# Kernel tuning notes

Hardware: AMD Instinct MI355X
Metric: run time of the kernel (lower is better)

Reference implementation:

```python
import jax, jax.numpy as jnp
import numpy as np

EMB = 1024
NHEAD = 16
HEAD_DIM = EMB // NHEAD  # 64
L = 2048
NEG = -1e30


def setup_inputs() -> dict:
    key = jax.random.key(0)
    ks = jax.random.split(key, 8)
    # xavier_uniform bound for square [EMB, EMB] matrices
    bound = float(np.sqrt(6.0 / (EMB + EMB)))
    def xavier(k):
        return jax.random.uniform(k, (EMB, EMB), jnp.float32, -bound, bound)
    return {
        "q": jax.random.normal(ks[0], (L, EMB), jnp.float32),
        "k": jax.random.normal(ks[1], (L, EMB), jnp.float32),
        "v": jax.random.normal(ks[2], (L, EMB), jnp.float32),
        "mask": jax.random.randint(ks[3], (NHEAD, L, L), 0, 2) > 0,
        "Wq": xavier(ks[4]),
        "Wk": xavier(ks[5]),
        "Wv": xavier(ks[6]),
        "Wo": xavier(ks[7]),
    }


def reference(q, k, v, mask, Wq, Wk, Wv, Wo):
    scaling = HEAD_DIM ** -0.5
    # F.linear(x, W) = x @ W.T ; reshape to [H, L, D]
    Q = (q @ Wq.T).reshape(L, NHEAD, HEAD_DIM).swapaxes(0, 1)
    K = (k @ Wk.T).reshape(L, NHEAD, HEAD_DIM).swapaxes(0, 1)
    V = (v @ Wv.T).reshape(L, NHEAD, HEAD_DIM).swapaxes(0, 1)
    scores = jnp.einsum("hld,hmd->hlm", Q, K) * scaling  # [H, L, L]
    scores = jnp.where(mask, jnp.asarray(NEG, scores.dtype), scores)
    p = jax.nn.softmax(scores, axis=-1)
    # attn_mask=True: multiplicative re-mask after softmax (custom path)
    p = p * (~mask).astype(p.dtype)
    # dropout is a no-op in eval mode
    attn_out = jnp.einsum("hlm,hmd->hld", p, V)  # [H, L, D]
    attn_out = attn_out.swapaxes(0, 1).reshape(L, EMB)
    return attn_out @ Wo.T
```

## Files before the change

### kernel.cpp

```cpp
#include <hip/hip_runtime.h>
#include <stdint.h>

#define EMB   1024
#define NHEAD 16
#define HDIM  64
#define SEQ   2048

typedef unsigned short ushort_t;
typedef unsigned int   uint32;
typedef __attribute__((ext_vector_type(8))) short bfrag;
typedef __attribute__((ext_vector_type(4))) float ffrag;

#define MFMA(a, b, c) __builtin_amdgcn_mfma_f32_16x16x32_bf16((a), (b), (c), 0, 0, 0)

__device__ inline ushort_t f2bf(float f) {
  uint32 u = __float_as_uint(f);
  u += 0x7FFFu + ((u >> 16) & 1u);
  return (ushort_t)(u >> 16);
}
__device__ inline uint32 pack2(float a, float b) {
  return (uint32)f2bf(a) | ((uint32)f2bf(b) << 16);
}

__device__ inline void glds16(const ushort_t* g, ushort_t* l) {
  __builtin_amdgcn_global_load_lds(
      (const __attribute__((address_space(1))) uint32*)(uintptr_t)g,
      (__attribute__((address_space(3))) uint32*)(uintptr_t)l, 16, 0, 0);
}

__global__ void detect_mask_kernel(const uint32* __restrict__ mw, int* __restrict__ flag) {
  uint32 w = mw[threadIdx.x];
  bool is4 = (w == 0u) || (w == 1u) || (w == 0x3F800000u);
  unsigned long long bad = __ballot(!is4);
  if (threadIdx.x == 0) flag[0] = (bad == 0ull) ? 1 : 0;
}

__global__ __launch_bounds__(256) void compress_mask(
    const void* __restrict__ maskp, const int* __restrict__ flag, ushort_t* __restrict__ bm)
{
  size_t t = (size_t)blockIdx.x * 256 + threadIdx.x;
  size_t row = t >> 7;
  int c16 = (int)(t & 127);
  size_t base = row * SEQ + (size_t)c16 * 16;
  ushort_t mv = 0;
  if (*flag) {
    const uint4* p = (const uint4*)((const uint32*)maskp + base);
    uint4 a0 = p[0], a1 = p[1], a2 = p[2], a3 = p[3];
    uint32 aw[16] = {a0.x,a0.y,a0.z,a0.w, a1.x,a1.y,a1.z,a1.w,
                     a2.x,a2.y,a2.z,a2.w, a3.x,a3.y,a3.z,a3.w};
    #pragma unroll
    for (int i = 0; i < 16; ++i) mv |= (ushort_t)((aw[i] != 0u) ? 1u : 0u) << i;
  } else {
    uint4 b0 = *(const uint4*)((const unsigned char*)maskp + base);
    uint32 bw[4] = {b0.x, b0.y, b0.z, b0.w};
    #pragma unroll
    for (int i = 0; i < 16; ++i)
      mv |= (ushort_t)((((bw[i >> 2] >> ((i & 3) * 8)) & 0xFFu) != 0u) ? 1u : 0u) << i;
  }
  bm[t] = mv;
}

__global__ __launch_bounds__(256) void cvt_all(
    const float4* __restrict__ q,  const float4* __restrict__ k,  const float4* __restrict__ v,
    const float4* __restrict__ wq, const float4* __restrict__ wk, const float4* __restrict__ wv,
    const float4* __restrict__ wo,
    uint2* __restrict__ qb,  uint2* __restrict__ kb,  uint2* __restrict__ vb,
    uint2* __restrict__ wqb, uint2* __restrict__ wkb, uint2* __restrict__ wvb,
    uint2* __restrict__ wob)
{
  int t = blockIdx.x * 256 + threadIdx.x;
  int s = blockIdx.y;
  const float4* src; uint2* dst; int n4;
  switch (s) {
    case 0: src = q;  dst = qb;  n4 = (SEQ * EMB) / 4; break;
    case 1: src = k;  dst = kb;  n4 = (SEQ * EMB) / 4; break;
    case 2: src = v;  dst = vb;  n4 = (SEQ * EMB) / 4; break;
    case 3: src = wq; dst = wqb; n4 = (EMB * EMB) / 4; break;
    case 4: src = wk; dst = wkb; n4 = (EMB * EMB) / 4; break;
    case 5: src = wv; dst = wvb; n4 = (EMB * EMB) / 4; break;
    default: src = wo; dst = wob; n4 = (EMB * EMB) / 4; break;
  }
  if (t >= n4) return;
  float4 f = src[t];
  uint2 o; o.x = pack2(f.x, f.y); o.y = pack2(f.z, f.w);
  dst[t] = o;
}

template<int MODE, int BN>
__device__ inline void gemm_body(const ushort_t* A, const ushort_t* B, void* Cp,
                                 int m0, int n0, ushort_t* As, ushort_t* Bs) {
  const int tid = threadIdx.x, lane = tid & 63, w = tid >> 6;
  const int wm = (w >> 1) * 64, wn = (w & 1) * (BN / 2);
  const int col = lane & 15, g = lane >> 4;
  constexpr int TN = BN / 32;
  constexpr int BIT = BN / 32;

  ffrag acc[4][TN] = {};

  for (int k0 = 0; k0 < EMB; k0 += 64) {
    __syncthreads();
    #pragma unroll
    for (int it = 0; it < 4; ++it) {
      int p = it * 256 + tid;
      int row = p >> 3, pc = p & 7;
      glds16(A + (size_t)(m0 + row) * EMB + k0 + (pc ^ (row & 7)) * 8, &As[p * 8]);
    }
    #pragma unroll
    for (int it = 0; it < BIT; ++it) {
      int p = it * 256 + tid;
      int row = p >> 3, pc = p & 7;
      glds16(B + (size_t)(n0 + row) * EMB + k0 + (pc ^ (row & 7)) * 8, &Bs[p * 8]);
    }
    __syncthreads();

    #pragma unroll
    for (int c = 0; c < 2; ++c) {
      bfrag av[4], bv[TN];
      #pragma unroll
      for (int t = 0; t < 4; ++t) {
        int ra = wm + t * 16 + col;
        av[t] = *(const bfrag*)&As[ra * 64 + ((c * 4 + g) ^ (ra & 7)) * 8];
      }
      #pragma unroll
      for (int t = 0; t < TN; ++t) {
        int rb = wn + t * 16 + col;
        bv[t] = *(const bfrag*)&Bs[rb * 64 + ((c * 4 + g) ^ (rb & 7)) * 8];
      }
      #pragma unroll
      for (int tm = 0; tm < 4; ++tm)
        #pragma unroll
        for (int tn = 0; tn < TN; ++tn)
          acc[tm][tn] = MFMA(av[tm], bv[tn], acc[tm][tn]);
    }
  }

  const int rbase = g * 4;
  #pragma unroll
  for (int tm = 0; tm < 4; ++tm)
    #pragma unroll
    for (int tn = 0; tn < TN; ++tn)
      #pragma unroll
      for (int r = 0; r < 4; ++r) {
        int m = m0 + wm + tm * 16 + rbase + r;
        int n = n0 + wn + tn * 16 + col;
        float vv = acc[tm][tn][r];
        if (MODE == 0) {
          ((ushort_t*)Cp)[((size_t)(n >> 6) * SEQ + m) * HDIM + (n & 63)] = f2bf(vv);
        } else if (MODE == 1) {
          ((ushort_t*)Cp)[((size_t)(m >> 6) * HDIM + (m & 63)) * SEQ + n] = f2bf(vv);
        } else {
          ((float*)Cp)[(size_t)m * EMB + n] = vv;
        }
      }
}

__global__ __launch_bounds__(256) void gemm_qkv(
    const ushort_t* __restrict__ qb, const ushort_t* __restrict__ kb, const ushort_t* __restrict__ vb,
    const ushort_t* __restrict__ Wqb, const ushort_t* __restrict__ Wkb, const ushort_t* __restrict__ Wvb,
    ushort_t* __restrict__ Qb, ushort_t* __restrict__ Kb, ushort_t* __restrict__ Vtb)
{
  __shared__ ushort_t As[128 * 64];
  __shared__ ushort_t Bs[64 * 64];
  const int z = blockIdx.y, bid = blockIdx.x;
  if (z == 0) {
    gemm_body<0, 64>(qb, Wqb, Qb, (bid >> 4) * 128, (bid & 15) * 64, As, Bs);
  } else if (z == 1) {
    gemm_body<0, 64>(kb, Wkb, Kb, (bid >> 4) * 128, (bid & 15) * 64, As, Bs);
  } else {
    gemm_body<1, 64>(Wvb, vb, Vtb, (bid >> 5) * 128, (bid & 31) * 64, As, Bs);
  }
}

__global__ __launch_bounds__(256) void gemm_out(
    const ushort_t* __restrict__ A, const ushort_t* __restrict__ B, float* __restrict__ C)
{
  __shared__ ushort_t As[128 * 64];
  __shared__ ushort_t Bs[64 * 64];
  gemm_body<2, 64>(A, B, (void*)C, blockIdx.y * 128, blockIdx.x * 64, As, Bs);
}

__global__ __launch_bounds__(256) void attn_mfma(
    const ushort_t* __restrict__ Qb,
    const ushort_t* __restrict__ Kb,
    const ushort_t* __restrict__ Vtb,
    const ushort_t* __restrict__ bm,
    ushort_t* __restrict__ attnb)
{
  __shared__ ushort_t KVs[2][2][64 * 64];
  __shared__ ushort_t Ps[4][16 * 72];

  const int tid  = threadIdx.x;
  const int lane = tid & 63;
  const int w    = tid >> 6;
  const int h    = blockIdx.y;
  const int l0   = blockIdx.x * 64;
  const int col  = lane & 15, g = lane >> 4, kg8 = g * 8, rbase = g * 4;

  ushort_t* pw = &Ps[w][0];

  {
    int rl = lane >> 2, seg = (lane & 3) * 16;
    const uint4* pq = (const uint4*)(Qb + ((size_t)h * SEQ + l0 + w * 16 + rl) * HDIM + seg);
    uint4 q0 = pq[0], q1 = pq[1];
    *(uint4*)&pw[rl * 72 + seg] = q0;
    *(uint4*)&pw[rl * 72 + seg + 8] = q1;
  }
  bfrag qf[2];
  qf[0] = *(const bfrag*)&pw[col * 72 + kg8];
  qf[1] = *(const bfrag*)&pw[col * 72 + 32 + kg8];

  auto stage_kv = [&](int kt_, int buf) {
    #pragma unroll
    for (int it = 0; it < 2; ++it) {
      int p = it * 256 + tid;
      int row = p >> 3, pc = p & 7;
      int sc = (pc ^ (row & 7)) * 8;
      glds16(Kb + ((size_t)h * SEQ + kt_ + row) * HDIM + sc, &KVs[buf][0][p * 8]);
      glds16(Vtb + ((size_t)h * HDIM + row) * SEQ + kt_ + sc, &KVs[buf][1][p * 8]);
    }
  };
  stage_kv(0, 0);

  const size_t bmbase = ((size_t)h * SEQ + l0 + w * 16 + (lane >> 2)) * 128 + (lane & 3);
  ushort_t mv_next = bm[bmbase];

  float lsum[4] = {0.f, 0.f, 0.f, 0.f};
  ffrag oacc[4] = {};

  for (int t = 0; t < 32; ++t) {
    const int buf = t & 1;
    __syncthreads();
    stage_kv(((t + 1) & 31) * 64, buf ^ 1);

    const ushort_t* Kc = &KVs[buf][0][0];
    const ushort_t* Vc = &KVs[buf][1][0];

    ushort_t mv = mv_next;
    mv_next = bm[bmbase + ((t + 1) & 31) * 4];

    ffrag s[4] = {};
    #pragma unroll
    for (int c = 0; c < 2; ++c)
      #pragma unroll
      for (int tn = 0; tn < 4; ++tn) {
        int row = tn * 16 + col;
        bfrag kf = *(const bfrag*)&Kc[row * 64 + ((c * 4 + g) ^ (row & 7)) * 8];
        s[tn] = MFMA(qf[c], kf, s[tn]);
      }

    #pragma unroll
    for (int r = 0; r < 4; ++r) {
      #pragma unroll
      for (int tn = 0; tn < 4; ++tn) {
        int m16 = __shfl((int)mv, (rbase + r) * 4 + tn, 64);
        bool msk = ((m16 >> col) & 1) != 0;
        float x = s[tn][r] * 0.125f;
        float p = msk ? 0.f : __expf(x);
        lsum[r] += p;
        pw[(rbase + r) * 72 + tn * 16 + col] = f2bf(p);
      }
    }

    #pragma unroll
    for (int c = 0; c < 2; ++c) {
      bfrag af = *(const bfrag*)&pw[col * 72 + c * 32 + kg8];
      #pragma unroll
      for (int tn = 0; tn < 4; ++tn) {
        int row = tn * 16 + col;
        bfrag vf = *(const bfrag*)&Vc[row * 64 + ((c * 4 + g) ^ (row & 7)) * 8];
        oacc[tn] = MFMA(af, vf, oacc[tn]);
      }
    }
  }

  float inv[4];
  #pragma unroll
  for (int r = 0; r < 4; ++r) {
    float s_ = lsum[r];
    #pragma unroll
    for (int off = 1; off < 16; off <<= 1) s_ += __shfl_xor(s_, off, 64);
    inv[r] = (s_ > 0.f) ? (1.0f / s_) : 0.0f;
  }
  #pragma unroll
  for (int tn = 0; tn < 4; ++tn)
    #pragma unroll
    for (int r = 0; r < 4; ++r) {
      int qg = l0 + w * 16 + rbase + r;
      attnb[(size_t)qg * EMB + h * HDIM + tn * 16 + col] = f2bf(oacc[tn][r] * inv[r]);
    }
}

extern "C" void kernel_launch(void* const* d_in, const int* in_sizes, int n_in,
                              void* d_out, int out_size, void* d_ws, size_t ws_size,
                              hipStream_t stream) {
  const float* q    = (const float*)d_in[0];
  const float* k    = (const float*)d_in[1];
  const float* v    = (const float*)d_in[2];
  const void*  mask =               d_in[3];
  const float* Wq   = (const float*)d_in[4];
  const float* Wk   = (const float*)d_in[5];
  const float* Wv   = (const float*)d_in[6];
  const float* Wo   = (const float*)d_in[7];

  char* ws = (char*)d_ws;
  const size_t MB = 1024 * 1024;
  ushort_t* qb    = (ushort_t*)(ws);
  ushort_t* kb    = (ushort_t*)(ws + 4  * MB);
  ushort_t* vb    = (ushort_t*)(ws + 8  * MB);
  ushort_t* Wqb   = (ushort_t*)(ws + 12 * MB);
  ushort_t* Wkb   = (ushort_t*)(ws + 14 * MB);
  ushort_t* Wvb   = (ushort_t*)(ws + 16 * MB);
  ushort_t* Wob   = (ushort_t*)(ws + 18 * MB);
  ushort_t* Qb    = (ushort_t*)(ws + 20 * MB);
  ushort_t* Kb    = (ushort_t*)(ws + 24 * MB);
  ushort_t* Vtb   = (ushort_t*)(ws + 28 * MB);
  int*      flag  = (int*)     (ws + 32 * MB);
  ushort_t* bmask = (ushort_t*)(ws + 33 * MB);
  ushort_t* attnb = qb;

  detect_mask_kernel<<<1, 64, 0, stream>>>((const uint32*)mask, flag);

  compress_mask<<<16384, 256, 0, stream>>>(mask, flag, bmask);

  cvt_all<<<dim3((SEQ * EMB / 4 + 255) / 256, 7), 256, 0, stream>>>(
      (const float4*)q, (const float4*)k, (const float4*)v,
      (const float4*)Wq, (const float4*)Wk, (const float4*)Wv, (const float4*)Wo,
      (uint2*)qb, (uint2*)kb, (uint2*)vb,
      (uint2*)Wqb, (uint2*)Wkb, (uint2*)Wvb, (uint2*)Wob);

  gemm_qkv<<<dim3(256, 3), 256, 0, stream>>>(qb, kb, vb, Wqb, Wkb, Wvb, Qb, Kb, Vtb);

  attn_mfma<<<dim3(SEQ / 64, NHEAD), 256, 0, stream>>>(Qb, Kb, Vtb, bmask, attnb);

  gemm_out<<<dim3(16, 16), 256, 0, stream>>>(attnb, Wob, (float*)d_out);
}
```

Baseline: 482.2 us.

## Split attention over key dimension and fuse mask compression into prep kernel

The attention kernel now splits the key sequence into two halves along a new grid z dimension. Each half writes unnormalized fp32 partial outputs and row sums, and a new merge kernel adds them, normalizes, and converts to bf16. This doubles the number of attention blocks to improve occupancy and parallelism. The mask detection, mask compression and input conversion kernels are folded into one prep launch to cut launch overhead. The cost is extra fp32 traffic for the partials (about 16MB written and read) and one more kernel launch.

```diff
diff --git a/kernel.cpp b/kernel.cpp
--- a/kernel.cpp
+++ b/kernel.cpp
@@ -28,62 +28,60 @@
       (__attribute__((address_space(3))) uint32*)(uintptr_t)l, 16, 0, 0);
 }
 
-__global__ void detect_mask_kernel(const uint32* __restrict__ mw, int* __restrict__ flag) {
-  uint32 w = mw[threadIdx.x];
-  bool is4 = (w == 0u) || (w == 1u) || (w == 0x3F800000u);
-  unsigned long long bad = __ballot(!is4);
-  if (threadIdx.x == 0) flag[0] = (bad == 0ull) ? 1 : 0;
-}
-
-__global__ __launch_bounds__(256) void compress_mask(
-    const void* __restrict__ maskp, const int* __restrict__ flag, ushort_t* __restrict__ bm)
-{
-  size_t t = (size_t)blockIdx.x * 256 + threadIdx.x;
-  size_t row = t >> 7;
-  int c16 = (int)(t & 127);
-  size_t base = row * SEQ + (size_t)c16 * 16;
-  ushort_t mv = 0;
-  if (*flag) {
-    const uint4* p = (const uint4*)((const uint32*)maskp + base);
-    uint4 a0 = p[0], a1 = p[1], a2 = p[2], a3 = p[3];
-    uint32 aw[16] = {a0.x,a0.y,a0.z,a0.w, a1.x,a1.y,a1.z,a1.w,
-                     a2.x,a2.y,a2.z,a2.w, a3.x,a3.y,a3.z,a3.w};
-    #pragma unroll
-    for (int i = 0; i < 16; ++i) mv |= (ushort_t)((aw[i] != 0u) ? 1u : 0u) << i;
-  } else {
-    uint4 b0 = *(const uint4*)((const unsigned char*)maskp + base);
-    uint32 bw[4] = {b0.x, b0.y, b0.z, b0.w};
-    #pragma unroll
-    for (int i = 0; i < 16; ++i)
-      mv |= (ushort_t)((((bw[i >> 2] >> ((i & 3) * 8)) & 0xFFu) != 0u) ? 1u : 0u) << i;
-  }
-  bm[t] = mv;
-}
-
-__global__ __launch_bounds__(256) void cvt_all(
+__global__ __launch_bounds__(256) void prep(
     const float4* __restrict__ q,  const float4* __restrict__ k,  const float4* __restrict__ v,
     const float4* __restrict__ wq, const float4* __restrict__ wk, const float4* __restrict__ wv,
-    const float4* __restrict__ wo,
+    const float4* __restrict__ wo, const void* __restrict__ maskp,
     uint2* __restrict__ qb,  uint2* __restrict__ kb,  uint2* __restrict__ vb,
     uint2* __restrict__ wqb, uint2* __restrict__ wkb, uint2* __restrict__ wvb,
-    uint2* __restrict__ wob)
-{
-  int t = blockIdx.x * 256 + threadIdx.x;
-  int s = blockIdx.y;
-  const float4* src; uint2* dst; int n4;
-  switch (s) {
-    case 0: src = q;  dst = qb;  n4 = (SEQ * EMB) / 4; break;
-    case 1: src = k;  dst = kb;  n4 = (SEQ * EMB) / 4; break;
-    case 2: src = v;  dst = vb;  n4 = (SEQ * EMB) / 4; break;
-    case 3: src = wq; dst = wqb; n4 = (EMB * EMB) / 4; break;
-    case 4: src = wk; dst = wkb; n4 = (EMB * EMB) / 4; break;
-    case 5: src = wv; dst = wvb; n4 = (EMB * EMB) / 4; break;
-    default: src = wo; dst = wob; n4 = (EMB * EMB) / 4; break;
-  }
-  if (t >= n4) return;
-  float4 f = src[t];
-  uint2 o; o.x = pack2(f.x, f.y); o.y = pack2(f.z, f.w);
-  dst[t] = o;
+    uint2* __restrict__ wob, ushort_t* __restrict__ bm)
+{
+  const int tid = threadIdx.x;
+  const int s = blockIdx.y;
+  if (s < 7) {
+    int t = blockIdx.x * 256 + tid;
+    const float4* src; uint2* dst; int n4;
+    switch (s) {
+      case 0: src = q;  dst = qb;  n4 = (SEQ * EMB) / 4; break;
+      case 1: src = k;  dst = kb;  n4 = (SEQ * EMB) / 4; break;
+      case 2: src = v;  dst = vb;  n4 = (SEQ * EMB) / 4; break;
+      case 3: src = wq; dst = wqb; n4 = (EMB * EMB) / 4; break;
+      case 4: src = wk; dst = wkb; n4 = (EMB * EMB) / 4; break;
+      case 5: src = wv; dst = wvb; n4 = (EMB * EMB) / 4; break;
+      default: src = wo; dst = wob; n4 = (EMB * EMB) / 4; break;
+    }
+    if (t >= n4) return;
+    float4 f = src[t];
+    uint2 o; o.x = pack2(f.x, f.y); o.y = pack2(f.z, f.w);
+    dst[t] = o;
+  } else {
+    uint32 w0 = ((const uint32*)maskp)[tid & 63];
+    bool is4 = (w0 == 0u) || (w0 == 1u) || (w0 == 0x3F800000u);
+    int use32 = (__ballot(!is4) == 0ull) ? 1 : 0;
+    #pragma unroll
+    for (int i = 0; i < 8; ++i) {
+      size_t t = (size_t)i * (2048 * 256) + (size_t)blockIdx.x * 256 + tid;
+      size_t row = t >> 7;
+      int c16 = (int)(t & 127);
+      size_t base = row * SEQ + (size_t)c16 * 16;
+      ushort_t mv = 0;
+      if (use32) {
+        const uint4* p = (const uint4*)((const uint32*)maskp + base);
+        uint4 a0 = p[0], a1 = p[1], a2 = p[2], a3 = p[3];
+        uint32 aw[16] = {a0.x,a0.y,a0.z,a0.w, a1.x,a1.y,a1.z,a1.w,
+                         a2.x,a2.y,a2.z,a2.w, a3.x,a3.y,a3.z,a3.w};
+        #pragma unroll
+        for (int j = 0; j < 16; ++j) mv |= (ushort_t)((aw[j] != 0u) ? 1u : 0u) << j;
+      } else {
+        uint4 b0 = *(const uint4*)((const unsigned char*)maskp + base);
+        uint32 bw[4] = {b0.x, b0.y, b0.z, b0.w};
+        #pragma unroll
+        for (int j = 0; j < 16; ++j)
+          mv |= (ushort_t)((((bw[j >> 2] >> ((j & 3) * 8)) & 0xFFu) != 0u) ? 1u : 0u) << j;
+      }
+      bm[t] = mv;
+    }
+  }
 }
 
 template<int MODE, int BN>
@@ -184,7 +182,8 @@
     const ushort_t* __restrict__ Kb,
     const ushort_t* __restrict__ Vtb,
     const ushort_t* __restrict__ bm,
-    ushort_t* __restrict__ attnb)
+    float* __restrict__ Op,
+    float* __restrict__ Ls)
 {
   __shared__ ushort_t KVs[2][2][64 * 64];
   __shared__ ushort_t Ps[4][16 * 72];
@@ -194,6 +193,7 @@
   const int w    = tid >> 6;
   const int h    = blockIdx.y;
   const int l0   = blockIdx.x * 64;
+  const int z    = blockIdx.z;
   const int col  = lane & 15, g = lane >> 4, kg8 = g * 8, rbase = g * 4;
 
   ushort_t* pw = &Ps[w][0];
@@ -219,24 +219,24 @@
       glds16(Vtb + ((size_t)h * HDIM + row) * SEQ + kt_ + sc, &KVs[buf][1][p * 8]);
     }
   };
-  stage_kv(0, 0);
+  stage_kv(z * 16 * 64, 0);
 
   const size_t bmbase = ((size_t)h * SEQ + l0 + w * 16 + (lane >> 2)) * 128 + (lane & 3);
-  ushort_t mv_next = bm[bmbase];
+  ushort_t mv_next = bm[bmbase + (size_t)(z * 16) * 4];
 
   float lsum[4] = {0.f, 0.f, 0.f, 0.f};
   ffrag oacc[4] = {};
 
-  for (int t = 0; t < 32; ++t) {
-    const int buf = t & 1;
+  for (int tt = 0; tt < 16; ++tt) {
+    const int buf = tt & 1;
     __syncthreads();
-    stage_kv(((t + 1) & 31) * 64, buf ^ 1);
+    stage_kv((z * 16 + ((tt + 1) & 15)) * 64, buf ^ 1);
 
     const ushort_t* Kc = &KVs[buf][0][0];
     const ushort_t* Vc = &KVs[buf][1][0];
 
     ushort_t mv = mv_next;
-    mv_next = bm[bmbase + ((t + 1) & 31) * 4];
+    mv_next = bm[bmbase + (size_t)(z * 16 + ((tt + 1) & 15)) * 4];
 
     ffrag s[4] = {};
     #pragma unroll
@@ -273,21 +273,44 @@
     }
   }
 
-  float inv[4];
+  float ls[4];
   #pragma unroll
   for (int r = 0; r < 4; ++r) {
     float s_ = lsum[r];
     #pragma unroll
     for (int off = 1; off < 16; off <<= 1) s_ += __shfl_xor(s_, off, 64);
-    inv[r] = (s_ > 0.f) ? (1.0f / s_) : 0.0f;
-  }
+    ls[r] = s_;
+  }
+  float* op = Op + (size_t)z * SEQ * EMB;
   #pragma unroll
   for (int tn = 0; tn < 4; ++tn)
     #pragma unroll
     for (int r = 0; r < 4; ++r) {
       int qg = l0 + w * 16 + rbase + r;
-      attnb[(size_t)qg * EMB + h * HDIM + tn * 16 + col] = f2bf(oacc[tn][r] * inv[r]);
-    }
+      op[(size_t)qg * EMB + h * HDIM + tn * 16 + col] = oacc[tn][r];
+    }
+  if (col == 0) {
+    #pragma unroll
+    for (int r = 0; r < 4; ++r)
+      Ls[((size_t)z * NHEAD + h) * SEQ + l0 + w * 16 + rbase + r] = ls[r];
+  }
+}
+
+__global__ __launch_bounds__(256) void merge_attn(
+    const float4* __restrict__ Op, const float* __restrict__ Ls, uint2* __restrict__ attnb)
+{
+  int t = blockIdx.x * 256 + threadIdx.x;
+  int qrow = t >> 8;
+  int h = (t & 255) >> 4;
+  float s0 = Ls[(size_t)h * SEQ + qrow];
+  float s1 = Ls[((size_t)NHEAD + h) * SEQ + qrow];
+  float ssum = s0 + s1;
+  float inv = (ssum > 0.f) ? (1.0f / ssum) : 0.0f;
+  float4 a = Op[t], b = Op[t + SEQ * EMB / 4];
+  uint2 r;
+  r.x = pack2((a.x + b.x) * inv, (a.y + b.y) * inv);
+  r.y = pack2((a.z + b.z) * inv, (a.w + b.w) * inv);
+  attnb[t] = r;
 }
 
 extern "C" void kernel_launch(void* const* d_in, const int* in_sizes, int n_in,
@@ -314,23 +337,22 @@
   ushort_t* Qb    = (ushort_t*)(ws + 20 * MB);
   ushort_t* Kb    = (ushort_t*)(ws + 24 * MB);
   ushort_t* Vtb   = (ushort_t*)(ws + 28 * MB);
-  int*      flag  = (int*)     (ws + 32 * MB);
   ushort_t* bmask = (ushort_t*)(ws + 33 * MB);
+  float*    Op    = (float*)   (ws + 44 * MB);
+  float*    Ls    = (float*)   (ws + 60 * MB);
   ushort_t* attnb = qb;
 
-  detect_mask_kernel<<<1, 64, 0, stream>>>((const uint32*)mask, flag);
-
-  compress_mask<<<16384, 256, 0, stream>>>(mask, flag, bmask);
-
-  cvt_all<<<dim3((SEQ * EMB / 4 + 255) / 256, 7), 256, 0, stream>>>(
+  prep<<<dim3(2048, 8), 256, 0, stream>>>(
       (const float4*)q, (const float4*)k, (const float4*)v,
-      (const float4*)Wq, (const float4*)Wk, (const float4*)Wv, (const float4*)Wo,
+      (const float4*)Wq, (const float4*)Wk, (const float4*)Wv, (const float4*)Wo, mask,
       (uint2*)qb, (uint2*)kb, (uint2*)vb,
-      (uint2*)Wqb, (uint2*)Wkb, (uint2*)Wvb, (uint2*)Wob);
+      (uint2*)Wqb, (uint2*)Wkb, (uint2*)Wvb, (uint2*)Wob, bmask);
 
   gemm_qkv<<<dim3(256, 3), 256, 0, stream>>>(qb, kb, vb, Wqb, Wkb, Wvb, Qb, Kb, Vtb);
 
-  attn_mfma<<<dim3(SEQ / 64, NHEAD), 256, 0, stream>>>(Qb, Kb, Vtb, bmask, attnb);
+  attn_mfma<<<dim3(SEQ / 64, NHEAD, 2), 256, 0, stream>>>(Qb, Kb, Vtb, bmask, Op, Ls);
+
+  merge_attn<<<2048, 256, 0, stream>>>((const float4*)Op, Ls, (uint2*)attnb);
 
   gemm_out<<<dim3(16, 16), 256, 0, stream>>>(attnb, Wob, (float*)d_out);
 }
```

Result: slower. 494.7 us (+2.6%).
